# Performance work log

Measured on AMD Instinct MI355X. Metric: run time of the kernel, lower is better.

The kernel has to match this reference:

```python
import jax, jax.numpy as jnp
import numpy as np

B, N, C, K = 16, 2000, 4, 8
EPS = 1e-5


def setup_inputs() -> dict:
    key = jax.random.key(0)
    ks = jax.random.split(key, 10)
    def p(k, shape, s=0.1):
        return jax.random.normal(k, shape, jnp.float32) * s
    return {
        "data": jax.random.normal(ks[0], (B, 1, N, C), jnp.float32),
        "x": jax.random.normal(ks[1], (B, 1, N, 4), jnp.float32),
        "w1a": p(ks[2], (128, C)), "b1a": jnp.zeros((128,), jnp.float32),
        "w1b": p(ks[3], (128, 128)), "b1b": jnp.zeros((128,), jnp.float32),
        "w2": p(ks[4], (128, 2 * C + 2)), "b2": jnp.zeros((128,), jnp.float32),
        "res_wa": p(ks[5], (4, 128, 128)), "res_ba": jnp.zeros((4, 128), jnp.float32),
        "res_wb": p(ks[6], (4, 128, 128)), "res_bb": jnp.zeros((4, 128), jnp.float32),
        "wl": p(ks[7], (1, 128)), "bl": jnp.zeros((1,), jnp.float32),
    }


def conv1x1(t, w, b):
    # t: [B, Cin, H, W], w: [Cout, Cin]
    return jnp.einsum('bchw,oc->bohw', t, w) + b[None, :, None, None]


def bn(t):
    # training-mode BatchNorm2d, gamma=1 beta=0 (default init)
    m = jnp.mean(t, axis=(0, 2, 3), keepdims=True)
    v = jnp.var(t, axis=(0, 2, 3), keepdims=True)
    return (t - m) * jax.lax.rsqrt(v + EPS)


def instn(t):
    # InstanceNorm2d, affine=False
    m = jnp.mean(t, axis=(2, 3), keepdims=True)
    v = jnp.var(t, axis=(2, 3), keepdims=True)
    return (t - m) * jax.lax.rsqrt(v + EPS)


def res_block(t, wa, ba, wb, bb):
    h = jax.nn.relu(bn(instn(conv1x1(t, wa, ba))))
    h = bn(instn(conv1x1(h, wb, bb)))
    return jax.nn.relu(h + t)


def knn_idx(f, k):
    # f: [B, D, N]; negative squared distance, top-(k+1), drop self
    xx = jnp.sum(f * f, axis=1)                        # [B, N]
    inner = jnp.einsum('bdn,bdm->bnm', f, f)           # [B, N, N]
    pd = 2.0 * inner - xx[:, :, None] - xx[:, None, :]
    idx = jax.lax.top_k(pd, k + 1)[1]                  # [B, N, k+1]
    return idx[:, :, 1:]


def graph_feature(f, idx):
    # f: [B, D, N], idx: [B, N, k] -> [B, 2D, N, k]
    xf = jnp.transpose(f, (0, 2, 1))                   # [B, N, D]
    nb = jax.vmap(lambda a, i: a[i])(xf, idx)          # [B, N, k, D]
    xt = xf[:, :, None, :]
    gf = jnp.concatenate([jnp.broadcast_to(xt, nb.shape), xt - nb], axis=-1)
    return jnp.transpose(gf, (0, 3, 1, 2))


def reference(data, x, w1a, b1a, w1b, b1b, w2, b2,
              res_wa, res_ba, res_wb, res_bb, wl, bl):
    n = data.shape[2]
    t = jnp.transpose(data, (0, 3, 2, 1))              # [B, C, N, 1]

    # self_attention
    h = conv1x1(t, w1a, b1a)
    h = jax.nn.relu(bn(h))
    h = conv1x1(h, w1b, b1b)[..., 0]                   # [B, 128, N]
    h = h / (jnp.linalg.norm(h, axis=1, keepdims=True) + 1e-5)
    A_rowsum = jnp.einsum('bcn,bcm->bm', h, h)         # sum_i A[i, j]
    D = (A_rowsum - 1.0) / n                           # [B, N] (eye subtraction)
    feat = jnp.concatenate(
        [t, jax.nn.relu(jnp.tanh(D))[:, None, :, None]], axis=1)  # [B, C+1, N, 1]

    f = feat[..., 0]                                   # [B, C+1, N]
    idx = knn_idx(f, K)
    g = graph_feature(f, idx)                          # [B, 2C+2, N, K]

    out = jax.nn.relu(bn(conv1x1(g, w2, b2)))          # [B, 128, N, K]
    out = jnp.max(out, axis=-1, keepdims=True)         # [B, 128, N, 1]

    for i in range(4):
        out = res_block(out, res_wa[i], res_ba[i], res_wb[i], res_bb[i])

    logit = conv1x1(out, wl, bl)[:, 0, :, 0]           # [B, N]

    # weighted 8-point
    weights = jax.nn.relu(jnp.tanh(logit))             # [B, N]
    xp = jnp.transpose(x[:, 0], (0, 2, 1))             # [B, 4, N]
    ones = jnp.ones_like(xp[:, 0])
    X = jnp.stack([xp[:, 2] * xp[:, 0], xp[:, 2] * xp[:, 1], xp[:, 2],
                   xp[:, 3] * xp[:, 0], xp[:, 3] * xp[:, 1], xp[:, 3],
                   xp[:, 0], xp[:, 1], ones], axis=1)  # [B, 9, N]
    X = jnp.transpose(X, (0, 2, 1))                    # [B, N, 9]
    XwX = jnp.einsum('bnp,bnq->bpq', X, weights[:, :, None] * X)  # [B, 9, 9]
    _, v = jnp.linalg.eigh(XwX)                        # ascending eigvals
    e_hat = v[:, :, 0]                                 # smallest-eig eigenvector
    e_hat = e_hat / jnp.linalg.norm(e_hat, axis=1, keepdims=True)

    return (D, logit, e_hat)
```

## Files before the change

### kernel.cpp

```cpp
#include <hip/hip_runtime.h>
#include <math.h>

#define BB 16
#define NN 2000
#define CH 128
#define KNN 8
#define JCH 8
#define JSZ 250

__device__ inline float wred(float v) {
    for (int off = 32; off > 0; off >>= 1) v += __shfl_down(v, off, 64);
    return v;
}

__global__ void k_conv1(const float* __restrict__ data, const float* __restrict__ w1a,
                        const float* __restrict__ b1a, float* __restrict__ c1) {
    int i = blockIdx.x * 256 + threadIdx.x;
    if (i >= BB * CH * NN) return;
    int n = i % NN;
    int rest = i / NN;
    int o = rest & 127;
    int b = rest >> 7;
    const float* dp = data + (b * NN + n) * 4;
    float acc = b1a[o];
    for (int c = 0; c < 4; ++c) acc += w1a[o * 4 + c] * dp[c];
    c1[i] = acc;
}

__global__ void k_chanstats(const float* __restrict__ src, float* __restrict__ chAB) {
    int o = blockIdx.x;
    int tid = threadIdx.x;
    float s = 0.f, ss = 0.f;
    for (int b = 0; b < BB; ++b) {
        const float* p = src + (b * CH + o) * NN;
        for (int n = tid; n < NN; n += 256) { float v = p[n]; s += v; ss += v * v; }
    }
    s = wred(s); ss = wred(ss);
    __shared__ float sh[8];
    int wid = tid >> 6, lane = tid & 63;
    if (lane == 0) { sh[wid] = s; sh[4 + wid] = ss; }
    __syncthreads();
    if (tid == 0) {
        float S0 = sh[0] + sh[1] + sh[2] + sh[3];
        float SS = sh[4] + sh[5] + sh[6] + sh[7];
        float m = S0 / (float)(BB * NN);
        float var = SS / (float)(BB * NN) - m * m;
        float a = rsqrtf(var + 1e-5f);
        chAB[o] = a;
        chAB[CH + o] = -m * a;
    }
}

__global__ __launch_bounds__(256) void k_gemm(const float* __restrict__ X, const float* __restrict__ W,
                                              const float* __restrict__ bias, float* __restrict__ Y,
                                              const float* __restrict__ ab, int mode) {
    int ot = blockIdx.x, by = blockIdx.y;
    int b = by >> 5, nt = by & 31;
    int n0 = nt * 64, o0 = ot * 64;
    int tid = threadIdx.x;
    int tx = tid & 15, ty = tid >> 4;
    __shared__ float Xs[32][64];
    __shared__ float Ws[32][68];
    float acc[4][4] = {};
    for (int jc = 0; jc < 4; ++jc) {
        for (int q = 0; q < 8; ++q) {
            int e = q * 256 + tid;
            int jj = e >> 6, nn = e & 63;
            int j = jc * 32 + jj, n = n0 + nn;
            float v = 0.f;
            if (n < NN) {
                v = X[(b * CH + j) * NN + n];
                if (mode == 1) v = fmaxf(ab[j] * v + ab[CH + j], 0.f);
                else if (mode == 2) { int bc = b * CH + j; v = fmaxf(ab[bc * 2] * v + ab[bc * 2 + 1], 0.f); }
            }
            Xs[jj][nn] = v;
        }
        for (int q = 0; q < 8; ++q) {
            int e = q * 256 + tid;
            int jj = e & 31, oo = e >> 5;
            Ws[jj][oo] = W[(o0 + oo) * CH + jc * 32 + jj];
        }
        __syncthreads();
        for (int jj = 0; jj < 32; ++jj) {
            float4 wv = *(const float4*)&Ws[jj][ty * 4];
            float4 xv = *(const float4*)&Xs[jj][tx * 4];
            float wva[4] = {wv.x, wv.y, wv.z, wv.w};
            float xva[4] = {xv.x, xv.y, xv.z, xv.w};
#pragma unroll
            for (int a = 0; a < 4; ++a)
#pragma unroll
                for (int bq = 0; bq < 4; ++bq) acc[a][bq] += wva[a] * xva[bq];
        }
        __syncthreads();
    }
    for (int a = 0; a < 4; ++a) {
        int o = o0 + ty * 4 + a;
        float bi = bias[o];
        for (int q = 0; q < 4; ++q) {
            int n = n0 + tx * 4 + q;
            if (n < NN) Y[(b * CH + o) * NN + n] = acc[a][q] + bi;
        }
    }
}

__global__ void k_invn(const float* __restrict__ h2, float* __restrict__ invn) {
    int b = blockIdx.x >> 3, chunk = blockIdx.x & 7;
    int n = chunk * 256 + threadIdx.x;
    if (n >= NN) return;
    float acc = 0.f;
    for (int c = 0; c < CH; ++c) { float v = h2[(b * CH + c) * NN + n]; acc += v * v; }
    invn[b * NN + n] = 1.f / (sqrtf(acc) + 1e-5f);
}

__global__ void k_S(const float* __restrict__ h2, const float* __restrict__ invn, float* __restrict__ Sv) {
    int row = blockIdx.x;
    int b = row >> 7;
    const float* p = h2 + row * NN;
    const float* iv = invn + b * NN;
    float s = 0.f;
    for (int n = threadIdx.x; n < NN; n += 256) s += p[n] * iv[n];
    s = wred(s);
    __shared__ float sh[4];
    int wid = threadIdx.x >> 6, lane = threadIdx.x & 63;
    if (lane == 0) sh[wid] = s;
    __syncthreads();
    if (threadIdx.x == 0) Sv[row] = sh[0] + sh[1] + sh[2] + sh[3];
}

__global__ void k_Df(const float* __restrict__ h2, const float* __restrict__ invn,
                     const float* __restrict__ Sv, const float* __restrict__ data,
                     float* __restrict__ outD, float* __restrict__ f5) {
    int b = blockIdx.x >> 3, chunk = blockIdx.x & 7;
    int n = chunk * 256 + threadIdx.x;
    if (n >= NN) return;
    float acc = 0.f;
    for (int c = 0; c < CH; ++c) acc += h2[(b * CH + c) * NN + n] * Sv[b * CH + c];
    float Ar = acc * invn[b * NN + n];
    float Dv = (Ar - 1.0f) / (float)NN;
    outD[b * NN + n] = Dv;
    const float* dp = data + (b * NN + n) * 4;
    for (int c = 0; c < 4; ++c) f5[(b * 5 + c) * NN + n] = dp[c];
    f5[(b * 5 + 4) * NN + n] = fmaxf(tanhf(Dv), 0.f);
}

__global__ __launch_bounds__(256) void k_knn_part(const float* __restrict__ f5,
                                                  float* __restrict__ pd, int* __restrict__ pj) {
    __shared__ float4 fs4[JSZ];
    __shared__ float fs1[JSZ];
    int jc = blockIdx.x, ic = blockIdx.y, b = blockIdx.z;
    int j0 = jc * JSZ;
    int tid = threadIdx.x;
    const float* fb = f5 + b * 5 * NN;
    for (int e = tid; e < JSZ; e += 256) {
        float4 v;
        v.x = fb[0 * NN + j0 + e];
        v.y = fb[1 * NN + j0 + e];
        v.z = fb[2 * NN + j0 + e];
        v.w = fb[3 * NN + j0 + e];
        fs4[e] = v;
        fs1[e] = fb[4 * NN + j0 + e];
    }
    __syncthreads();
    int i = ic * 256 + tid;
    if (i >= NN) return;
    float fi0 = fb[i], fi1 = fb[NN + i], fi2 = fb[2 * NN + i], fi3 = fb[3 * NN + i], fi4 = fb[4 * NN + i];
    float bd[8]; int bj[8];
#pragma unroll
    for (int q = 0; q < 8; ++q) { bd[q] = 1e30f; bj[q] = 0x7fffffff; }
    for (int jj = 0; jj < JSZ; ++jj) {
        float4 fj = fs4[jj];
        float fj4 = fs1[jj];
        int j = j0 + jj;
        float d0 = fi0 - fj.x, d1 = fi1 - fj.y, d2 = fi2 - fj.z;
        float d3 = fi3 - fj.w, d4 = fi4 - fj4;
        float d = d0 * d0 + d1 * d1 + d2 * d2 + d3 * d3 + d4 * d4;
        if (j != i && d < bd[7]) {
            float cd = d; int cj = j;
#pragma unroll
            for (int q = 0; q < 8; ++q) {
                bool lt = cd < bd[q];
                float td = lt ? bd[q] : cd;
                int tj = lt ? bj[q] : cj;
                bd[q] = lt ? cd : bd[q];
                bj[q] = lt ? cj : bj[q];
                cd = td; cj = tj;
            }
        }
    }
    long base = ((long)(b * NN + i) * JCH + jc) * 8;
#pragma unroll
    for (int q = 0; q < 8; ++q) { pd[base + q] = bd[q]; pj[base + q] = bj[q]; }
}

__global__ __launch_bounds__(256) void k_knn_merge(const float* __restrict__ pd, const int* __restrict__ pj,
                                                   int* __restrict__ idxb) {
    int s = blockIdx.x * 256 + threadIdx.x;
    if (s >= BB * NN) return;
    const float* dl = pd + (long)s * JCH * 8;
    const int* jl = pj + (long)s * JCH * 8;
    int ptr[JCH];
#pragma unroll
    for (int c = 0; c < JCH; ++c) ptr[c] = 0;
    for (int q = 0; q < 8; ++q) {
        float best = 1e38f; int bestj = 0x7fffffff; int bc = 0;
#pragma unroll
        for (int c = 0; c < JCH; ++c) {
            if (ptr[c] < 8) {
                float d = dl[c * 8 + ptr[c]];
                int j = jl[c * 8 + ptr[c]];
                if (d < best || (d == best && j < bestj)) { best = d; bestj = j; bc = c; }
            }
        }
        idxb[s * 8 + q] = bestj;
        ++ptr[bc];
    }
}

__global__ __launch_bounds__(256) void k_gstats(const float* __restrict__ f5, const int* __restrict__ idxb,
                                                double* __restrict__ gacc) {
    int s = blockIdx.x * 256 + threadIdx.x;
    float acc[65];
#pragma unroll
    for (int q = 0; q < 65; ++q) acc[q] = 0.f;
    if (s < BB * NN) {
        int b = s / NN, n = s - b * NN;
        float fo[5];
#pragma unroll
        for (int c = 0; c < 5; ++c) fo[c] = f5[(b * 5 + c) * NN + n];
        float sd[5] = {0, 0, 0, 0, 0};
        float sdd[15];
#pragma unroll
        for (int q = 0; q < 15; ++q) sdd[q] = 0.f;
        for (int k = 0; k < 8; ++k) {
            int j = idxb[s * 8 + k];
            float df[5];
#pragma unroll
            for (int c = 0; c < 5; ++c) df[c] = fo[c] - f5[(b * 5 + c) * NN + j];
#pragma unroll
            for (int c = 0; c < 5; ++c) sd[c] += df[c];
            int t = 0;
#pragma unroll
            for (int c = 0; c < 5; ++c)
#pragma unroll
                for (int d2 = c; d2 < 5; ++d2) { sdd[t] += df[c] * df[d2]; ++t; }
        }
#pragma unroll
        for (int c = 0; c < 5; ++c) { acc[c] = 8.f * fo[c]; acc[5 + c] = sd[c]; }
        int t = 10, sc = 0;
        for (int p = 0; p < 10; ++p)
            for (int q = p; q < 10; ++q) {
                float v;
                if (q < 5) v = 8.f * fo[p] * fo[q];
                else if (p < 5) v = fo[p] * sd[q - 5];
                else { v = sdd[sc]; ++sc; }
                acc[t++] = v;
            }
    }
#pragma unroll 1
    for (int q = 0; q < 65; ++q) {
        float v = acc[q];
        for (int off = 32; off > 0; off >>= 1) v += __shfl_down(v, off, 64);
        acc[q] = v;
    }
    __shared__ float sh[4][65];
    int lane = threadIdx.x & 63, wid = threadIdx.x >> 6;
    if (lane == 0) {
        for (int q = 0; q < 65; ++q) sh[wid][q] = acc[q];
    }
    __syncthreads();
    if (threadIdx.x < 65) {
        float tot = sh[0][threadIdx.x] + sh[1][threadIdx.x] + sh[2][threadIdx.x] + sh[3][threadIdx.x];
        atomicAdd(&gacc[threadIdx.x], (double)tot);
    }
}

__global__ void k_gfinal(const double* __restrict__ gacc, const float* __restrict__ w2,
                         const float* __restrict__ b2, float* __restrict__ g2ab) {
    int o = threadIdx.x;
    if (o >= 128) return;
    double inv = 1.0 / (double)(BB * NN * 8);
    double Wr[10];
    for (int c = 0; c < 10; ++c) Wr[c] = (double)w2[o * 10 + c];
    double gm[10];
    for (int c = 0; c < 10; ++c) gm[c] = gacc[c] * inv;
    double b0 = (double)b2[o];
    double mean = b0;
    for (int c = 0; c < 10; ++c) mean += Wr[c] * gm[c];
    double e2 = b0 * b0 + 2.0 * b0 * (mean - b0);
    int t = 10;
    for (int p = 0; p < 10; ++p)
        for (int q = p; q < 10; ++q) {
            double G = gacc[t] * inv; ++t;
            double contrib = Wr[p] * Wr[q] * G;
            e2 += (p == q) ? contrib : 2.0 * contrib;
        }
    double var = e2 - mean * mean;
    double a = 1.0 / sqrt(var + 1e-5);
    g2ab[o] = (float)a;
    g2ab[128 + o] = (float)(-mean * a);
}

__global__ __launch_bounds__(256) void k_graphconv(const float* __restrict__ f5, const int* __restrict__ idxb,
                                                   const float* __restrict__ w2, const float* __restrict__ b2,
                                                   const float* __restrict__ g2ab, float* __restrict__ x0) {
    __shared__ float ws[1280], bs[128];
    __shared__ float fo_s[16][5], fnb_s[16][8][5];
    __shared__ int idxs[16][8];
    int b = blockIdx.x / 125, tile = blockIdx.x % 125;
    int nbase = tile * 16;
    int tid = threadIdx.x;
    for (int e = tid; e < 1280; e += 256) ws[e] = w2[e];
    if (tid < 128) bs[tid] = b2[tid];
    if (tid < 128) { int nn = tid >> 3, k = tid & 7; idxs[nn][k] = idxb[(b * NN + nbase + nn) * 8 + k]; }
    if (tid >= 128 && tid < 208) { int e = tid - 128; int nn = e / 5, c = e % 5; fo_s[nn][c] = f5[(b * 5 + c) * NN + nbase + nn]; }
    __syncthreads();
    for (int e = tid; e < 640; e += 256) {
        int nn = e / 40, r = e % 40, k = r / 5, c = r % 5;
        fnb_s[nn][k][c] = f5[(b * 5 + c) * NN + idxs[nn][k]];
    }
    __syncthreads();
    int nn = tid & 15, og = tid >> 4;
    float fo[5];
#pragma unroll
    for (int c = 0; c < 5; ++c) fo[c] = fo_s[nn][c];
    for (int oo = 0; oo < 8; ++oo) {
        int o = og * 8 + oo;
        float base = bs[o];
        float wn[5];
#pragma unroll
        for (int c = 0; c < 5; ++c) {
            float w1 = ws[o * 10 + c], w5 = ws[o * 10 + 5 + c];
            base += (w1 + w5) * fo[c];
            wn[c] = w5;
        }
        float mx = -1e30f;
        for (int k = 0; k < 8; ++k) {
            float v = base;
#pragma unroll
            for (int c = 0; c < 5; ++c) v -= wn[c] * fnb_s[nn][k][c];
            mx = fmaxf(mx, v);
        }
        float y = fmaxf(g2ab[o] * mx + g2ab[128 + o], 0.f);
        x0[(b * CH + o) * NN + nbase + nn] = y;
    }
}

__global__ void k_rowstats(const float* __restrict__ src, float* __restrict__ stats) {
    int row = blockIdx.x;
    const float* p = src + row * NN;
    float s = 0.f, ss = 0.f;
    for (int n = threadIdx.x; n < NN; n += 256) { float v = p[n]; s += v; ss += v * v; }
    s = wred(s); ss = wred(ss);
    __shared__ float sh[8];
    int wid = threadIdx.x >> 6, lane = threadIdx.x & 63;
    if (lane == 0) { sh[wid] = s; sh[4 + wid] = ss; }
    __syncthreads();
    if (threadIdx.x == 0) {
        float S0 = sh[0] + sh[1] + sh[2] + sh[3];
        float SS = sh[4] + sh[5] + sh[6] + sh[7];
        float m = S0 / (float)NN;
        float var = SS / (float)NN - m * m;
        stats[row * 2] = m;
        stats[row * 2 + 1] = var;
    }
}

__global__ void k_finalize(const float* __restrict__ stats, float* __restrict__ ab) {
    int c = threadIdx.x;
    if (c >= 128) return;
    float acc = 0.f;
    for (int b = 0; b < BB; ++b) { float var = stats[(b * CH + c) * 2 + 1]; acc += var / (var + 1e-5f); }
    float vc = acc / (float)BB;
    float sc = rsqrtf(vc + 1e-5f);
    for (int b = 0; b < BB; ++b) {
        float m = stats[(b * CH + c) * 2];
        float var = stats[(b * CH + c) * 2 + 1];
        float a = rsqrtf(var + 1e-5f) * sc;
        ab[(b * CH + c) * 2] = a;
        ab[(b * CH + c) * 2 + 1] = -m * a;
    }
}

__global__ void k_resadd(const float* __restrict__ Bm, const float* __restrict__ ab,
                         const float* __restrict__ x, float* __restrict__ y) {
    int i = blockIdx.x * 256 + threadIdx.x;
    if (i >= BB * CH * NN) return;
    int bc = i / NN;
    float v = ab[bc * 2] * Bm[i] + ab[bc * 2 + 1] + x[i];
    y[i] = fmaxf(v, 0.f);
}

__global__ void k_logit(const float* __restrict__ x4, const float* __restrict__ wl,
                        const float* __restrict__ bl, float* __restrict__ outLogit) {
    int b = blockIdx.x >> 3, chunk = blockIdx.x & 7;
    int n = chunk * 256 + threadIdx.x;
    if (n >= NN) return;
    float acc = 0.f;
    for (int c = 0; c < CH; ++c) acc += wl[c] * x4[(b * CH + c) * NN + n];
    outLogit[b * NN + n] = acc + bl[0];
}

__global__ __launch_bounds__(256) void k_xwx(const float* __restrict__ logit, const float* __restrict__ x_in,
                                             float* __restrict__ XwX) {
    int b = blockIdx.x;
    int tid = threadIdx.x;
    float a[45];
#pragma unroll
    for (int q = 0; q < 45; ++q) a[q] = 0.f;
    for (int n = tid; n < NN; n += 256) {
        float lg = logit[b * NN + n];
        float w = fmaxf(tanhf(lg), 0.f);
        const float* xp = x_in + (b * NN + n) * 4;
        float px = xp[0], py = xp[1], z = xp[2], wq = xp[3];
        float X9[9] = {z * px, z * py, z, wq * px, wq * py, wq, px, py, 1.f};
        int t = 0;
#pragma unroll
        for (int p = 0; p < 9; ++p) {
            float wp = w * X9[p];
#pragma unroll
            for (int q = p; q < 9; ++q) { a[t] += wp * X9[q]; ++t; }
        }
    }
#pragma unroll 1
    for (int q = 0; q < 45; ++q) {
        float v = a[q];
        for (int off = 32; off > 0; off >>= 1) v += __shfl_down(v, off, 64);
        a[q] = v;
    }
    __shared__ float sh[4][45];
    int lane = tid & 63, wid = tid >> 6;
    if (lane == 0) {
        for (int q = 0; q < 45; ++q) sh[wid][q] = a[q];
    }
    __syncthreads();
    if (tid < 45) XwX[b * 45 + tid] = sh[0][tid] + sh[1][tid] + sh[2][tid] + sh[3][tid];
}

__device__ __forceinline__ float lgetf(float reg, int i) {
    return __int_as_float(__builtin_amdgcn_readlane(__float_as_int(reg), i));
}
__device__ __forceinline__ float wsum64(float v) {
    for (int off = 32; off > 0; off >>= 1) v += __shfl_xor(v, off, 64);
    return v;
}

__device__ inline float slapy2_f(float x, float y) {
    float xa = fabsf(x), ya = fabsf(y);
    float w = fmaxf(xa, ya), z = fminf(xa, ya);
    if (z == 0.f) return w;
    float q = z / w;
    return w * sqrtf(1.f + q * q);
}

__device__ inline void slartg_f(float f, float g, float& c, float& s, float& r) {
    if (g == 0.f) { c = 1.f; s = 0.f; r = f; }
    else if (f == 0.f) { c = 0.f; s = (g > 0.f ? 1.f : -1.f); r = fabsf(g); }
    else {
        float d = sqrtf(f * f + g * g);
        c = fabsf(f) / d;
        r = (f >= 0.f) ? d : -d;
        s = g / r;
    }
}

__device__ void slaev2_f(float a, float b, float c, float& rt1, float& rt2, float& cs1, float& sn1) {
    float sm = a + c, df = a - c;
    float adf = fabsf(df), tb = b + b, ab = fabsf(tb);
    float acmx, acmn;
    if (fabsf(a) > fabsf(c)) { acmx = a; acmn = c; } else { acmx = c; acmn = a; }
    float rt;
    if (adf > ab) { float q = ab / adf; rt = adf * sqrtf(1.f + q * q); }
    else if (adf < ab) { float q = adf / ab; rt = ab * sqrtf(1.f + q * q); }
    else rt = ab * sqrtf(2.f);
    int sgn1;
    if (sm < 0.f) { rt1 = 0.5f * (sm - rt); sgn1 = -1; rt2 = (acmx / rt1) * acmn - (b / rt1) * b; }
    else if (sm > 0.f) { rt1 = 0.5f * (sm + rt); sgn1 = 1; rt2 = (acmx / rt1) * acmn - (b / rt1) * b; }
    else { rt1 = 0.5f * rt; rt2 = -0.5f * rt; sgn1 = 1; }
    float cs; int sgn2;
    if (df >= 0.f) { cs = df + rt; sgn2 = 1; } else { cs = df - rt; sgn2 = -1; }
    float acs = fabsf(cs);
    if (acs > ab) {
        float ct = -tb / cs;
        sn1 = 1.f / sqrtf(1.f + ct * ct);
        cs1 = ct * sn1;
    } else {
        if (ab == 0.f) { cs1 = 1.f; sn1 = 0.f; }
        else { float tn = -cs / tb; cs1 = 1.f / sqrtf(1.f + tn * tn); sn1 = tn * cs1; }
    }
    if (sgn1 == sgn2) { float tn = cs1; cs1 = -sn1; sn1 = tn; }
}

#define ROTLOG_MAX 2560

__global__ __launch_bounds__(64) void k_eigh(const float* __restrict__ XwX, float* __restrict__ out_e) {
    __shared__ float Am[81];
    __shared__ float rcl[ROTLOG_MAX], rsl[ROTLOG_MAX];
    __shared__ int rjl[ROTLOG_MAX];
    int bb = blockIdx.x;
    int lane = threadIdx.x;
#define AA(i, j) Am[(i) * 9 + (j)]
#define DGET(i) lgetf(dreg, (i))
#define DSET(i, v) do { float _v = (v); dreg = (lane == (i)) ? _v : dreg; } while (0)
#define EGET(i) lgetf(ereg, (i))
#define ESET(i, v) do { float _v = (v); ereg = (lane == (i)) ? _v : ereg; } while (0)
    {
        const float* src = XwX + bb * 45;
        for (int e2 = lane; e2 < 81; e2 += 64) {
            int r0 = e2 / 9, c0 = e2 % 9;
            int a0 = r0 < c0 ? r0 : c0, b0 = r0 < c0 ? c0 : r0;
            int t = a0 * 9 - (a0 * (a0 - 1)) / 2 + (b0 - a0);
            Am[e2] = src[t];
        }
    }
    __syncthreads();
    float dreg = 0.f, ereg = 0.f, treg = 0.f;
    int cnt = 0;
    for (int i = 0; i < 8; ++i) {
        float alpha = AA(i + 1, i);
        float xn2 = 0.f;
        for (int j = i + 2; j < 9; ++j) xn2 += AA(j, i) * AA(j, i);
        float taui;
        if (xn2 == 0.f) { taui = 0.f; ESET(i, alpha); }
        else {
            float xnorm = sqrtf(xn2);
            float beta = slapy2_f(alpha, xnorm);
            beta = (alpha >= 0.f) ? -beta : beta;
            taui = (beta - alpha) / beta;
            float scl = 1.f / (alpha - beta);
            for (int j = i + 2; j < 9; ++j) AA(j, i) *= scl;
            ESET(i, beta);
            float p[9], w[9];
            for (int j = i + 1; j < 9; ++j) {
                float acc = AA(j, i + 1);
                for (int k2 = i + 2; k2 < 9; ++k2) acc += AA(j, k2) * AA(k2, i);
                p[j] = taui * acc;
            }
            float dot = p[i + 1];
            for (int j = i + 2; j < 9; ++j) dot += p[j] * AA(j, i);
            float alpha2 = -0.5f * taui * dot;
            w[i + 1] = p[i + 1] + alpha2;
            for (int j = i + 2; j < 9; ++j) w[j] = p[j] + alpha2 * AA(j, i);
            for (int j = i + 1; j < 9; ++j) {
                float vj = (j == i + 1) ? 1.f : AA(j, i);
                for (int k2 = i + 1; k2 < 9; ++k2) {
                    float vk = (k2 == i + 1) ? 1.f : AA(k2, i);
                    float upd = AA(j, k2) - (vj * w[k2] + w[j] * vk);
                    __syncthreads();
                    if (lane == 0) AA(j, k2) = upd;
                    __syncthreads();
                }
            }
        }
        treg = (lane == i) ? taui : treg;
    }
    dreg = (lane < 9) ? Am[lane * 10] : 0.f;
    const float eps = 5.9604645e-08f;
    const float eps2 = 3.5527137e-15f;
    const float safmin = 1.17549435e-38f;
    const int n = 9;
    int nmaxit = n * 30, jtot = 0;
    int l1 = 0;
    while (l1 <= n - 1) {
        if (l1 > 0) ESET(l1 - 1, 0.f);
        int m = n - 1;
        for (int mm = l1; mm <= n - 2; ++mm) {
            float tst = fabsf(EGET(mm));
            if (tst == 0.f) { m = mm; break; }
            if (tst <= (sqrtf(fabsf(DGET(mm))) * sqrtf(fabsf(DGET(mm + 1)))) * eps) { ESET(mm, 0.f); m = mm; break; }
        }
        int l = l1, lsv = l, lend = m, lendsv = lend;
        l1 = m + 1;
        if (lend == l) continue;
        if (fabsf(DGET(lend)) < fabsf(DGET(l))) { lend = lsv; l = lendsv; }
        if (lend > l) {
            for (;;) {
                int m2 = lend;
                if (l != lend) {
                    for (int mm = l; mm <= lend - 1; ++mm) {
                        float em = EGET(mm);
                        float tst = em * em;
                        if (tst <= (eps2 * fabsf(DGET(mm))) * fabsf(DGET(mm + 1)) + safmin) { m2 = mm; break; }
                    }
                }
                if (m2 < lend) ESET(m2, 0.f);
                float p = DGET(l);
                if (m2 == l) { DSET(l, p); ++l; if (l <= lend) continue; else break; }
                if (m2 == l + 1) {
                    float rt1, rt2, c, s;
                    slaev2_f(DGET(l), EGET(l), DGET(l + 1), rt1, rt2, c, s);
                    if (lane == 0) { rcl[cnt] = c; rsl[cnt] = s; rjl[cnt] = l; }
                    ++cnt;
                    DSET(l, rt1); DSET(l + 1, rt2); ESET(l, 0.f); l += 2;
                    if (l <= lend) continue; else break;
                }
                if (jtot == nmaxit) break;
                ++jtot;
                float g = (DGET(l + 1) - p) / (2.f * EGET(l));
                float r = slapy2_f(g, 1.f);
                g = DGET(m2) - p + EGET(l) / (g + (g >= 0.f ? fabsf(r) : -fabsf(r)));
                float s = 1.f, c = 1.f;
                p = 0.f;
                for (int i = m2 - 1; i >= l; --i) {
                    float ei = EGET(i);
                    float f = s * ei, bq = c * ei;
                    slartg_f(g, f, c, s, r);
                    if (i != m2 - 1) ESET(i + 1, r);
                    g = DGET(i + 1) - p;
                    r = (DGET(i) - g) * s + 2.f * c * bq;
                    p = s * r;
                    DSET(i + 1, g + p);
                    g = c * r - bq;
                    if (lane == 0) { rcl[cnt] = c; rsl[cnt] = -s; rjl[cnt] = i; }
                    ++cnt;
                }
                DSET(l, DGET(l) - p);
                ESET(l, g);
            }
        } else {
            for (;;) {
                int m2 = lend;
                if (l != lend) {
                    for (int mm = l; mm >= lend + 1; --mm) {
                        float em = EGET(mm - 1);
                        float tst = em * em;
                        if (tst <= (eps2 * fabsf(DGET(mm))) * fabsf(DGET(mm - 1)) + safmin) { m2 = mm; break; }
                    }
                }
                if (m2 > lend) ESET(m2 - 1, 0.f);
                float p = DGET(l);
                if (m2 == l) { DSET(l, p); --l; if (l >= lend) continue; else break; }
                if (m2 == l - 1) {
                    float rt1, rt2, c, s;
                    slaev2_f(DGET(l - 1), EGET(l - 1), DGET(l), rt1, rt2, c, s);
                    if (lane == 0) { rcl[cnt] = c; rsl[cnt] = s; rjl[cnt] = l - 1; }
                    ++cnt;
                    DSET(l - 1, rt1); DSET(l, rt2); ESET(l - 1, 0.f); l -= 2;
                    if (l >= lend) continue; else break;
                }
                if (jtot == nmaxit) break;
                ++jtot;
                float g = (DGET(l - 1) - p) / (2.f * EGET(l - 1));
                float r = slapy2_f(g, 1.f);
                g = DGET(m2) - p + EGET(l - 1) / (g + (g >= 0.f ? fabsf(r) : -fabsf(r)));
                float s = 1.f, c = 1.f;
                p = 0.f;
                for (int i = m2; i <= l - 1; ++i) {
                    float ei = EGET(i);
                    float f = s * ei, bq = c * ei;
                    slartg_f(g, f, c, s, r);
                    if (i != m2) ESET(i - 1, r);
                    g = DGET(i) - p;
                    r = (DGET(i + 1) - g) * s + 2.f * c * bq;
                    p = s * r;
                    DSET(i, g + p);
                    g = c * r - bq;
                    if (lane == 0) { rcl[cnt] = c; rsl[cnt] = s; rjl[cnt] = i; }
                    ++cnt;
                }
                DSET(l, DGET(l) - p);
                ESET(l - 1, g);
            }
        }
    }
    __syncthreads();
    int permreg = lane;
    for (int ii = 1; ii < 9; ++ii) {
        int i = ii - 1, kk = i;
        float p = DGET(i);
        for (int j = ii; j < 9; ++j) {
            float dj = DGET(j);
            if (dj < p) { kk = j; p = dj; }
        }
        if (kk != i) {
            float di = DGET(i);
            DSET(kk, di);
            DSET(i, p);
            int pi = __builtin_amdgcn_readlane(permreg, i);
            int pk = __builtin_amdgcn_readlane(permreg, kk);
            permreg = (lane == i) ? pk : permreg;
            permreg = (lane == kk) ? pi : permreg;
        }
    }
    int kcol = __builtin_amdgcn_readlane(permreg, 0);
    float v0reg = (lane == kcol) ? 1.f : 0.f;
    for (int t = cnt - 1; t >= 0; --t) {
        float c = rcl[t], s = rsl[t];
        int j = rjl[t];
        float a = lgetf(v0reg, j);
        float b2 = lgetf(v0reg, j + 1);
        float nj = c * a - s * b2;
        float nj1 = s * a + c * b2;
        v0reg = (lane == j) ? nj : v0reg;
        v0reg = (lane == j + 1) ? nj1 : v0reg;
    }
    for (int i = 7; i >= 0; --i) {
        float ti = lgetf(treg, i);
        if (ti == 0.f) continue;
        float avi = (lane >= i + 2 && lane <= 8) ? Am[lane * 9 + i] : 0.f;
        float contrib = 0.f;
        if (lane == i + 1) contrib = v0reg;
        else if (lane >= i + 2 && lane <= 8) contrib = avi * v0reg;
        float dot = wsum64(contrib) * ti;
        if (lane == i + 1) v0reg -= dot;
        else if (lane >= i + 2 && lane <= 8) v0reg -= avi * dot;
    }
    float sq = (lane < 9) ? v0reg * v0reg : 0.f;
    float nrm = sqrtf(wsum64(sq));
    if (lane < 9) out_e[bb * 9 + lane] = v0reg / nrm;
#undef AA
#undef DGET
#undef DSET
#undef EGET
#undef ESET
}

extern "C" void kernel_launch(void* const* d_in, const int* in_sizes, int n_in,
                              void* d_out, int out_size, void* d_ws, size_t ws_size,
                              hipStream_t stream) {
    const float* data = (const float*)d_in[0];
    const float* x_in = (const float*)d_in[1];
    const float* w1a = (const float*)d_in[2];
    const float* b1a = (const float*)d_in[3];
    const float* w1b = (const float*)d_in[4];
    const float* b1b = (const float*)d_in[5];
    const float* w2 = (const float*)d_in[6];
    const float* b2 = (const float*)d_in[7];
    const float* res_wa = (const float*)d_in[8];
    const float* res_ba = (const float*)d_in[9];
    const float* res_wb = (const float*)d_in[10];
    const float* res_bb = (const float*)d_in[11];
    const float* wl = (const float*)d_in[12];
    const float* bl = (const float*)d_in[13];
    float* out = (float*)d_out;

    double* gacc = (double*)d_ws;
    float* xwx = (float*)((char*)d_ws + 1024);
    float* fbase = (float*)((char*)d_ws + 8192);
    float* big0 = fbase;
    float* big1 = big0 + BB * CH * NN;
    float* big2 = big1 + BB * CH * NN;
    float* tbuf = big2 + BB * CH * NN;
    float* f5 = tbuf + BB * 4 * NN;
    float* invn = f5 + BB * 5 * NN;
    float* Sv = invn + BB * NN;
    int* idxb = (int*)(Sv + BB * CH);
    float* chAB = (float*)(idxb + BB * NN * 8);
    float* stA = chAB + 256;
    float* abA = stA + BB * CH * 2;
    float* stB = abA + BB * CH * 2;
    float* abB = stB + BB * CH * 2;
    float* g2ab = abB + BB * CH * 2;
    float* knn_pd = big2;
    int* knn_pj = (int*)(big2 + BB * NN * JCH * 8);

    hipMemsetAsync(d_ws, 0, 1024, stream);

    k_conv1<<<16000, 256, 0, stream>>>(data, w1a, b1a, big0);
    k_chanstats<<<128, 256, 0, stream>>>(big0, chAB);
    k_gemm<<<dim3(2, 512), 256, 0, stream>>>(big0, w1b, b1b, big1, chAB, 1);
    k_invn<<<128, 256, 0, stream>>>(big1, invn);
    k_S<<<2048, 256, 0, stream>>>(big1, invn, Sv);
    k_Df<<<128, 256, 0, stream>>>(big1, invn, Sv, data, out, f5);
    k_knn_part<<<dim3(JCH, 8, BB), 256, 0, stream>>>(f5, knn_pd, knn_pj);
    k_knn_merge<<<125, 256, 0, stream>>>(knn_pd, knn_pj, idxb);
    k_gstats<<<125, 256, 0, stream>>>(f5, idxb, gacc);
    k_gfinal<<<1, 128, 0, stream>>>(gacc, w2, b2, g2ab);
    k_graphconv<<<2000, 256, 0, stream>>>(f5, idxb, w2, b2, g2ab, big0);

    float* xb = big0;
    float* hb = big1;
    for (int i = 0; i < 4; ++i) {
        k_gemm<<<dim3(2, 512), 256, 0, stream>>>(xb, res_wa + i * CH * CH, res_ba + i * CH, hb, nullptr, 0);
        k_rowstats<<<2048, 256, 0, stream>>>(hb, stA);
        k_finalize<<<1, 128, 0, stream>>>(stA, abA);
        k_gemm<<<dim3(2, 512), 256, 0, stream>>>(hb, res_wb + i * CH * CH, res_bb + i * CH, big2, abA, 2);
        k_rowstats<<<2048, 256, 0, stream>>>(big2, stB);
        k_finalize<<<1, 128, 0, stream>>>(stB, abB);
        k_resadd<<<16000, 256, 0, stream>>>(big2, abB, xb, hb);
        float* tmp = xb; xb = hb; hb = tmp;
    }

    k_logit<<<128, 256, 0, stream>>>(xb, wl, bl, out + BB * NN);
    k_xwx<<<16, 256, 0, stream>>>(out + BB * NN, x_in, xwx);
    k_eigh<<<16, 64, 0, stream>>>(xwx, out + 2 * BB * NN);
}
```

Before: 835.1 us.

## Fuse knn merge with gstats, fold finalize into rowstats via atomic counters

Merges the kNN merge kernel into the graph-stats kernel so the selected neighbor indices stay in registers instead of making a round trip through global memory. Folds each BN finalize step into the row-stats kernel: the last block per channel, detected with an atomic counter plus threadfence, computes the scale and shift. This removes 9 kernel launches in total. The kNN scan is also unrolled by two to expose more ILP, and the workspace memset grows to zero the counters.

```diff
diff --git a/kernel.cpp b/kernel.cpp
--- a/kernel.cpp
+++ b/kernel.cpp
@@ -167,62 +167,63 @@
     float bd[8]; int bj[8];
 #pragma unroll
     for (int q = 0; q < 8; ++q) { bd[q] = 1e30f; bj[q] = 0x7fffffff; }
-    for (int jj = 0; jj < JSZ; ++jj) {
-        float4 fj = fs4[jj];
-        float fj4 = fs1[jj];
-        int j = j0 + jj;
-        float d0 = fi0 - fj.x, d1 = fi1 - fj.y, d2 = fi2 - fj.z;
-        float d3 = fi3 - fj.w, d4 = fi4 - fj4;
-        float d = d0 * d0 + d1 * d1 + d2 * d2 + d3 * d3 + d4 * d4;
-        if (j != i && d < bd[7]) {
-            float cd = d; int cj = j;
-#pragma unroll
-            for (int q = 0; q < 8; ++q) {
-                bool lt = cd < bd[q];
-                float td = lt ? bd[q] : cd;
-                int tj = lt ? bj[q] : cj;
-                bd[q] = lt ? cd : bd[q];
-                bj[q] = lt ? cj : bj[q];
-                cd = td; cj = tj;
-            }
-        }
+    auto ins = [&](float cd, int cj) {
+#pragma unroll
+        for (int q = 0; q < 8; ++q) {
+            bool lt = cd < bd[q];
+            float td = lt ? bd[q] : cd;
+            int tj = lt ? bj[q] : cj;
+            bd[q] = lt ? cd : bd[q];
+            bj[q] = lt ? cj : bj[q];
+            cd = td; cj = tj;
+        }
+    };
+    for (int jj = 0; jj < JSZ; jj += 2) {
+        float4 fja = fs4[jj];
+        float fa4 = fs1[jj];
+        float4 fjb = fs4[jj + 1];
+        float fb4 = fs1[jj + 1];
+        float a0 = fi0 - fja.x, a1 = fi1 - fja.y, a2 = fi2 - fja.z, a3 = fi3 - fja.w, a4 = fi4 - fa4;
+        float da = a0 * a0 + a1 * a1 + a2 * a2 + a3 * a3 + a4 * a4;
+        float b0 = fi0 - fjb.x, b1 = fi1 - fjb.y, b2 = fi2 - fjb.z, b3 = fi3 - fjb.w, b4 = fi4 - fb4;
+        float db = b0 * b0 + b1 * b1 + b2 * b2 + b3 * b3 + b4 * b4;
+        int ja = j0 + jj, jb = j0 + jj + 1;
+        if (ja != i && da < bd[7]) ins(da, ja);
+        if (jb != i && db < bd[7]) ins(db, jb);
     }
     long base = ((long)(b * NN + i) * JCH + jc) * 8;
 #pragma unroll
     for (int q = 0; q < 8; ++q) { pd[base + q] = bd[q]; pj[base + q] = bj[q]; }
 }
 
-__global__ __launch_bounds__(256) void k_knn_merge(const float* __restrict__ pd, const int* __restrict__ pj,
-                                                   int* __restrict__ idxb) {
+__global__ __launch_bounds__(256) void k_knn_gstats(const float* __restrict__ pd, const int* __restrict__ pj,
+                                                    const float* __restrict__ f5, int* __restrict__ idxb,
+                                                    double* __restrict__ gacc) {
     int s = blockIdx.x * 256 + threadIdx.x;
-    if (s >= BB * NN) return;
-    const float* dl = pd + (long)s * JCH * 8;
-    const int* jl = pj + (long)s * JCH * 8;
-    int ptr[JCH];
-#pragma unroll
-    for (int c = 0; c < JCH; ++c) ptr[c] = 0;
-    for (int q = 0; q < 8; ++q) {
-        float best = 1e38f; int bestj = 0x7fffffff; int bc = 0;
-#pragma unroll
-        for (int c = 0; c < JCH; ++c) {
-            if (ptr[c] < 8) {
-                float d = dl[c * 8 + ptr[c]];
-                int j = jl[c * 8 + ptr[c]];
-                if (d < best || (d == best && j < bestj)) { best = d; bestj = j; bc = c; }
-            }
-        }
-        idxb[s * 8 + q] = bestj;
-        ++ptr[bc];
-    }
-}
-
-__global__ __launch_bounds__(256) void k_gstats(const float* __restrict__ f5, const int* __restrict__ idxb,
-                                                double* __restrict__ gacc) {
-    int s = blockIdx.x * 256 + threadIdx.x;
+    int bjv[8];
     float acc[65];
 #pragma unroll
     for (int q = 0; q < 65; ++q) acc[q] = 0.f;
     if (s < BB * NN) {
+        const float* dl = pd + (long)s * JCH * 8;
+        const int* jl = pj + (long)s * JCH * 8;
+        int ptr[JCH];
+#pragma unroll
+        for (int c = 0; c < JCH; ++c) ptr[c] = 0;
+        for (int q = 0; q < 8; ++q) {
+            float best = 1e38f; int bestj = 0x7fffffff; int bc = 0;
+#pragma unroll
+            for (int c = 0; c < JCH; ++c) {
+                if (ptr[c] < 8) {
+                    float d = dl[c * 8 + ptr[c]];
+                    int j = jl[c * 8 + ptr[c]];
+                    if (d < best || (d == best && j < bestj)) { best = d; bestj = j; bc = c; }
+                }
+            }
+            bjv[q] = bestj;
+            idxb[s * 8 + q] = bestj;
+            ++ptr[bc];
+        }
         int b = s / NN, n = s - b * NN;
         float fo[5];
 #pragma unroll
@@ -232,7 +233,7 @@
 #pragma unroll
         for (int q = 0; q < 15; ++q) sdd[q] = 0.f;
         for (int k = 0; k < 8; ++k) {
-            int j = idxb[s * 8 + k];
+            int j = bjv[k];
             float df[5];
 #pragma unroll
             for (int c = 0; c < 5; ++c) df[c] = fo[c] - f5[(b * 5 + c) * NN + j];
@@ -345,8 +346,10 @@
     }
 }
 
-__global__ void k_rowstats(const float* __restrict__ src, float* __restrict__ stats) {
+__global__ void k_rowfin2(const float* __restrict__ src, float* __restrict__ stats,
+                          float* __restrict__ ab, int* __restrict__ cnt) {
     int row = blockIdx.x;
+    int c = row & 127;
     const float* p = src + row * NN;
     float s = 0.f, ss = 0.f;
     for (int n = threadIdx.x; n < NN; n += 256) { float v = p[n]; s += v; ss += v * v; }
@@ -362,22 +365,22 @@
         float var = SS / (float)NN - m * m;
         stats[row * 2] = m;
         stats[row * 2 + 1] = var;
-    }
-}
-
-__global__ void k_finalize(const float* __restrict__ stats, float* __restrict__ ab) {
-    int c = threadIdx.x;
-    if (c >= 128) return;
-    float acc = 0.f;
-    for (int b = 0; b < BB; ++b) { float var = stats[(b * CH + c) * 2 + 1]; acc += var / (var + 1e-5f); }
-    float vc = acc / (float)BB;
-    float sc = rsqrtf(vc + 1e-5f);
-    for (int b = 0; b < BB; ++b) {
-        float m = stats[(b * CH + c) * 2];
-        float var = stats[(b * CH + c) * 2 + 1];
-        float a = rsqrtf(var + 1e-5f) * sc;
-        ab[(b * CH + c) * 2] = a;
-        ab[(b * CH + c) * 2 + 1] = -m * a;
+        __threadfence();
+        int old = atomicAdd(&cnt[c], 1);
+        if (old == BB - 1) {
+            __threadfence();
+            float acc = 0.f;
+            for (int b = 0; b < BB; ++b) { float v2 = stats[(b * CH + c) * 2 + 1]; acc += v2 / (v2 + 1e-5f); }
+            float vc = acc / (float)BB;
+            float sc = rsqrtf(vc + 1e-5f);
+            for (int b = 0; b < BB; ++b) {
+                float m2 = stats[(b * CH + c) * 2];
+                float v2 = stats[(b * CH + c) * 2 + 1];
+                float a2 = rsqrtf(v2 + 1e-5f) * sc;
+                ab[(b * CH + c) * 2] = a2;
+                ab[(b * CH + c) * 2 + 1] = -m2 * a2;
+            }
+        }
     }
 }
 
@@ -735,7 +738,8 @@
 
     double* gacc = (double*)d_ws;
     float* xwx = (float*)((char*)d_ws + 1024);
-    float* fbase = (float*)((char*)d_ws + 8192);
+    int* counters = (int*)((char*)d_ws + 4096);
+    float* fbase = (float*)((char*)d_ws + 16384);
     float* big0 = fbase;
     float* big1 = big0 + BB * CH * NN;
     float* big2 = big1 + BB * CH * NN;
@@ -753,7 +757,7 @@
     float* knn_pd = big2;
     int* knn_pj = (int*)(big2 + BB * NN * JCH * 8);
 
-    hipMemsetAsync(d_ws, 0, 1024, stream);
+    hipMemsetAsync(d_ws, 0, 16384, stream);
 
     k_conv1<<<16000, 256, 0, stream>>>(data, w1a, b1a, big0);
     k_chanstats<<<128, 256, 0, stream>>>(big0, chAB);
@@ -762,8 +766,7 @@
     k_S<<<2048, 256, 0, stream>>>(big1, invn, Sv);
     k_Df<<<128, 256, 0, stream>>>(big1, invn, Sv, data, out, f5);
     k_knn_part<<<dim3(JCH, 8, BB), 256, 0, stream>>>(f5, knn_pd, knn_pj);
-    k_knn_merge<<<125, 256, 0, stream>>>(knn_pd, knn_pj, idxb);
-    k_gstats<<<125, 256, 0, stream>>>(f5, idxb, gacc);
+    k_knn_gstats<<<125, 256, 0, stream>>>(knn_pd, knn_pj, f5, idxb, gacc);
     k_gfinal<<<1, 128, 0, stream>>>(gacc, w2, b2, g2ab);
     k_graphconv<<<2000, 256, 0, stream>>>(f5, idxb, w2, b2, g2ab, big0);
 
@@ -771,11 +774,9 @@
     float* hb = big1;
     for (int i = 0; i < 4; ++i) {
         k_gemm<<<dim3(2, 512), 256, 0, stream>>>(xb, res_wa + i * CH * CH, res_ba + i * CH, hb, nullptr, 0);
-        k_rowstats<<<2048, 256, 0, stream>>>(hb, stA);
-        k_finalize<<<1, 128, 0, stream>>>(stA, abA);
+        k_rowfin2<<<2048, 256, 0, stream>>>(hb, stA, abA, counters + (i * 2) * 128);
         k_gemm<<<dim3(2, 512), 256, 0, stream>>>(hb, res_wb + i * CH * CH, res_bb + i * CH, big2, abA, 2);
-        k_rowstats<<<2048, 256, 0, stream>>>(big2, stB);
-        k_finalize<<<1, 128, 0, stream>>>(stB, abB);
+        k_rowfin2<<<2048, 256, 0, stream>>>(big2, stB, abB, counters + (i * 2 + 1) * 128);
         k_resadd<<<16000, 256, 0, stream>>>(big2, abB, xb, hb);
         float* tmp = xb; xb = hb; hb = tmp;
     }
```

After: 1.061 ms. +27.1%, slower.
